# Optimization experiments

Measured on AMD Instinct MI355X. Metric: run time of the kernel, lower is better.

## Reference

```python
import jax, jax.numpy as jnp
import numpy as np
import math

B, S, HID = 1, 4096, 2048
NH, NKV, DH = 8, 1, 256
ROPE_BASE = 10000.0


def setup_inputs() -> dict:
    key = jax.random.key(0)
    ks = jax.random.split(key, 5)
    sc = 0.02
    return {
        "hidden_states": jax.random.normal(ks[0], (B, S, HID), dtype=jnp.float32),
        "position_ids": jnp.arange(S, dtype=jnp.int32)[None, :].repeat(B, axis=0),
        "wq": jax.random.normal(ks[1], (HID, NH * DH), dtype=jnp.float32) * sc,
        "wk": jax.random.normal(ks[2], (HID, NKV * DH), dtype=jnp.float32) * sc,
        "wv": jax.random.normal(ks[3], (HID, NKV * DH), dtype=jnp.float32) * sc,
        "wo": jax.random.normal(ks[4], (NH * DH, HID), dtype=jnp.float32) * sc,
    }


def _rope_cos_sin(position_ids, dtype):
    # inv_freq: [DH/2]
    inv_freq = 1.0 / (ROPE_BASE ** (jnp.arange(0, DH, 2, dtype=jnp.float32) / DH))
    # freqs: [B, S, DH/2]
    freqs = position_ids.astype(jnp.float32)[:, :, None] * inv_freq[None, None, :]
    emb = jnp.concatenate([freqs, freqs], axis=-1)  # [B, S, DH]
    return jnp.cos(emb).astype(dtype), jnp.sin(emb).astype(dtype)


def _rotate_half(x):
    x1, x2 = x[..., : DH // 2], x[..., DH // 2 :]
    return jnp.concatenate([-x2, x1], axis=-1)


def reference(hidden_states, position_ids, wq, wk, wv, wo):
    bsz, q_len, _ = hidden_states.shape
    dtype = hidden_states.dtype

    # QKV projections (bias=False)
    q = (hidden_states @ wq).reshape(bsz, q_len, NH, DH).transpose(0, 2, 1, 3)   # [B,NH,S,DH]
    k = (hidden_states @ wk).reshape(bsz, q_len, NKV, DH).transpose(0, 2, 1, 3)  # [B,NKV,S,DH]
    v = (hidden_states @ wv).reshape(bsz, q_len, NKV, DH).transpose(0, 2, 1, 3)  # [B,NKV,S,DH]

    # RoPE (unsqueeze_dim=1 -> broadcast over heads)
    cos, sin = _rope_cos_sin(position_ids, dtype)
    cos, sin = cos[:, None, :, :], sin[:, None, :, :]  # [B,1,S,DH]
    q = q * cos + _rotate_half(q) * sin
    k = k * cos + _rotate_half(k) * sin

    # GQA: k/v broadcast over the NH head dim via matmul broadcasting (repeat_kv)
    scores = jnp.matmul(q, jnp.swapaxes(k, -1, -2)) / math.sqrt(DH)  # [B,NH,S,S]

    # additive causal mask (0 on/below diagonal, -inf-ish above)
    neg = jnp.finfo(jnp.float32).min
    causal = jnp.where(
        jnp.tril(jnp.ones((q_len, q_len), dtype=bool)), 0.0, neg
    ).astype(jnp.float32)[None, None, :, :]
    scores = scores + causal

    probs = jax.nn.softmax(scores.astype(jnp.float32), axis=-1).astype(dtype)
    attn = jnp.matmul(probs, v)  # [B,NH,S,DH] (v broadcasts over NH)

    attn = attn.transpose(0, 2, 1, 3).reshape(bsz, q_len, NH * DH)
    return attn @ wo
```

## Files before the change

### kernel.cpp

```cpp
#include <hip/hip_runtime.h>
#include <hip/hip_bf16.h>

typedef __bf16 bf16;
typedef __attribute__((ext_vector_type(8))) __bf16 bf16x8;
typedef __attribute__((ext_vector_type(4))) float f32x4;

#define S_LEN  4096
#define HIDDEN 2048
#define N_HEADS 8
#define D_HEAD 256
#define QKV_N  2560
#define NEG_BIG (-1e30f)
#define MFIX 8.0f

#define OFF_WQKVT 0u
#define OFF_WOT   10485760u
#define OFF_QKV   18874368u
#define OFF_VT    39845888u
#define OFF_AOUT  41943040u
#define OFF_FLAG  58720256u
#define WS_NEED   58720320u
#define OFF_PBUF  0u
#define OFF_LBUF  8388608u

__global__ __launch_bounds__(256) void detect_dtype(const unsigned short* __restrict__ w,
                                                    int* __restrict__ flag) {
  __shared__ int bad;
  if (threadIdx.x == 0) bad = 0;
  __syncthreads();
  int local = 0;
  for (int i = threadIdx.x; i < 4096; i += 256) {
    int e = (w[i] >> 7) & 0xFF;
    if (e >= 130) local = 1;
  }
  if (local) atomicOr(&bad, 1);
  __syncthreads();
  if (threadIdx.x == 0) *flag = bad;
}

__device__ __forceinline__ bf16x8 load8(const void* p, size_t idx, bool f32) {
  if (f32) {
    const float* q = (const float*)p + idx;
    bf16x8 r;
#pragma unroll
    for (int j = 0; j < 8; ++j) r[j] = (bf16)q[j];
    return r;
  }
  return *(const bf16x8*)((const bf16*)p + idx);
}

__global__ __launch_bounds__(256) void cvt_hs(const void* __restrict__ hs,
                                              bf16* __restrict__ dst,
                                              const int* __restrict__ flag) {
  bool f32 = (*flag != 0);
  size_t i = ((size_t)blockIdx.x * 256 + threadIdx.x) * 8;
  *(bf16x8*)(dst + i) = load8(hs, i, f32);
}

__device__ __forceinline__ void transpose_tile64(const void* __restrict__ src, size_t sbase,
                                                 int sld, bool f32,
                                                 bf16* __restrict__ dst, int dld,
                                                 bf16 (*T)[72]) {
  int tid = threadIdx.x;
  int r  = tid >> 2;
  int c4 = (tid & 3) * 16;
  *(bf16x8*)(&T[r][c4])     = load8(src, sbase + (size_t)r * sld + c4, f32);
  *(bf16x8*)(&T[r][c4 + 8]) = load8(src, sbase + (size_t)r * sld + c4 + 8, f32);
  __syncthreads();
  bf16x8 v0, v1;
#pragma unroll
  for (int j = 0; j < 8; ++j) { v0[j] = T[c4 + j][r]; v1[j] = T[c4 + 8 + j][r]; }
  *(bf16x8*)(dst + (size_t)r * dld + c4)     = v0;
  *(bf16x8*)(dst + (size_t)r * dld + c4 + 8) = v1;
}

__global__ __launch_bounds__(256) void build_wqkvT(const void* __restrict__ wq,
                                                   const void* __restrict__ wk,
                                                   const void* __restrict__ wv,
                                                   bf16* __restrict__ dst,
                                                   const int* __restrict__ flag) {
  __shared__ __align__(16) bf16 T[64][72];
  bool f32 = (*flag != 0);
  int n0 = blockIdx.x * 64;
  int k0 = blockIdx.y * 64;
  const void* src; int ld, c0;
  if (n0 < 2048)      { src = wq; ld = 2048; c0 = n0; }
  else if (n0 < 2304) { src = wk; ld = 256;  c0 = n0 - 2048; }
  else                { src = wv; ld = 256;  c0 = n0 - 2304; }
  transpose_tile64(src, (size_t)k0 * ld + c0, ld, f32,
                   dst + (size_t)n0 * HIDDEN + k0, HIDDEN, T);
}

__global__ __launch_bounds__(256) void transpose_any(const void* __restrict__ src, int sbase,
                                                     int sld,
                                                     bf16* __restrict__ dst, int dld,
                                                     const int* __restrict__ flag) {
  __shared__ __align__(16) bf16 T[64][72];
  bool f32 = flag && (*flag != 0);
  int c0 = blockIdx.x * 64;
  int r0 = blockIdx.y * 64;
  transpose_tile64(src, (size_t)sbase + (size_t)r0 * sld + c0, sld, f32,
                   dst + (size_t)c0 * dld + r0, dld, T);
}

__device__ __forceinline__ void gload16(const bf16* g, bf16* l) {
  __builtin_amdgcn_global_load_lds((__attribute__((address_space(1))) void*)(void*)g,
                                   (__attribute__((address_space(3))) void*)(void*)l,
                                   16, 0, 0);
}

__global__ __launch_bounds__(256) void gemm_bk64(const bf16* __restrict__ A,
                                                 const bf16* __restrict__ BT,
                                                 void* __restrict__ C,
                                                 int M, int N, int K,
                                                 const int* __restrict__ cflag) {
  __shared__ __align__(16) bf16 As[2][128 * 64];
  __shared__ __align__(16) bf16 Bs[2][128 * 64];
  bool cf32 = cflag && (*cflag != 0);
  int tid  = threadIdx.x;
  int w = tid >> 6, lane = tid & 63;
  int quad = lane >> 4, l16 = lane & 15;

  int nx = gridDim.x;
  int nwg = nx * gridDim.y;
  int bid = blockIdx.y * nx + blockIdx.x;
  int swz = (bid & 7) * (nwg >> 3) + (bid >> 3);
  int bm = (swz / nx) * 128, bn = (swz % nx) * 128;
  int wm = (w >> 1) * 64, wn = (w & 1) * 64;

  int lr = lane >> 3, lc = lane & 7;
  int scol = ((lc ^ lr) << 3);
  const bf16* Ag[4]; const bf16* Bg[4];
#pragma unroll
  for (int j = 0; j < 4; ++j) {
    int row = (w * 4 + j) * 8 + lr;
    Ag[j] = A  + (size_t)(bm + row) * K + scol;
    Bg[j] = BT + (size_t)(bn + row) * K + scol;
  }

  int nIter = K >> 6;
#pragma unroll
  for (int j = 0; j < 4; ++j) {
    gload16(Ag[j], &As[0][(w * 4 + j) * 512]);
    gload16(Bg[j], &Bs[0][(w * 4 + j) * 512]);
  }
  __syncthreads();

  int cA = ((quad    ) ^ (l16 & 7)) << 3;
  int cB = ((quad + 4) ^ (l16 & 7)) << 3;

  f32x4 acc[4][4] = {};
  for (int kt = 0; kt < nIter; ++kt) {
    int cur = kt & 1;
    if (kt + 1 < nIter) {
      int nxt = cur ^ 1;
      int koff = (kt + 1) << 6;
#pragma unroll
      for (int j = 0; j < 4; ++j) {
        gload16(Ag[j] + koff, &As[nxt][(w * 4 + j) * 512]);
        gload16(Bg[j] + koff, &Bs[nxt][(w * 4 + j) * 512]);
      }
    }
    const bf16* Ab = &As[cur][0];
    const bf16* Bb = &Bs[cur][0];
#pragma unroll
    for (int h = 0; h < 2; ++h) {
      int cc = h ? cB : cA;
      bf16x8 af[4], bfr[4];
#pragma unroll
      for (int mt = 0; mt < 4; ++mt)
        af[mt] = *(const bf16x8*)(Ab + (wm + mt * 16 + l16) * 64 + cc);
#pragma unroll
      for (int nt = 0; nt < 4; ++nt)
        bfr[nt] = *(const bf16x8*)(Bb + (wn + nt * 16 + l16) * 64 + cc);
#pragma unroll
      for (int mt = 0; mt < 4; ++mt)
#pragma unroll
        for (int nt = 0; nt < 4; ++nt)
          acc[mt][nt] = __builtin_amdgcn_mfma_f32_16x16x32_bf16(af[mt], bfr[nt],
                                                                acc[mt][nt], 0, 0, 0);
    }
    __syncthreads();
  }

#pragma unroll
  for (int mt = 0; mt < 4; ++mt)
#pragma unroll
    for (int nt = 0; nt < 4; ++nt)
#pragma unroll
      for (int r = 0; r < 4; ++r) {
        int row = bm + wm + mt * 16 + quad * 4 + r;
        int col = bn + wn + nt * 16 + l16;
        size_t off = (size_t)row * N + col;
        float v = acc[mt][nt][r];
        if (cf32) ((float*)C)[off] = v;
        else      ((bf16*)C)[off] = (bf16)v;
      }
}

__global__ __launch_bounds__(256) void rope_kernel(bf16* __restrict__ qkv,
                                                   const int* __restrict__ pos) {
  int s = blockIdx.x;
  float p = (float)pos[s];
  bf16* row = qkv + (size_t)s * QKV_N;
  for (int i = threadIdx.x; i < 9 * 128; i += 256) {
    int h = i >> 7, d = i & 127;
    float inv = __expf(-(float)d * (9.210340371976184f / 128.0f));
    float th = p * inv;
    float sn, c;
    sincosf(th, &sn, &c);
    c  = (float)(bf16)c;
    sn = (float)(bf16)sn;
    bf16* x = row + ((h < 8) ? h * 256 : 2048);
    float x1 = (float)x[d], x2 = (float)x[d + 128];
    x[d]       = (bf16)(x1 * c - x2 * sn);
    x[d + 128] = (bf16)(x2 * c + x1 * sn);
  }
}

__device__ __forceinline__ void stage_kv(const bf16* __restrict__ qkv,
                                         const bf16* __restrict__ VT,
                                         bf16* __restrict__ kb, bf16* __restrict__ vb,
                                         int kv0, int w, int lane) {
#pragma unroll
  for (int i = 0; i < 4; ++i) {
    int seg = w * 4 + i;
    int rK = seg * 2 + (lane >> 5);
    int sK = (lane & 31) ^ (rK & 31);
    gload16(qkv + (size_t)(kv0 + rK) * QKV_N + 2048 + sK * 8, kb + seg * 512);
    int rV = seg * 8 + (lane >> 3);
    int sV = (lane & 7) ^ (rV & 7);
    gload16(VT + (size_t)rV * S_LEN + kv0 + sV * 8, vb + seg * 512);
  }
}

__global__ __launch_bounds__(512, 2) void attn_kernel(const bf16* __restrict__ qkv,
                                                      const bf16* __restrict__ VT,
                                                      bf16* __restrict__ aout,
                                                      bf16* __restrict__ pbuf,
                                                      float* __restrict__ lbuf) {
  __shared__ __align__(16) bf16 Ks[2][64 * 256];
  __shared__ __align__(16) bf16 Vs[2][256 * 64];
  __shared__ __align__(16) bf16 Pl[8][16][72];
  int tid  = threadIdx.x;
  int w = tid >> 6, lane = tid & 63;
  int quad = lane >> 4, l16 = lane & 15;
  int bx   = blockIdx.x;
  int head = bx & 7;
  int t    = bx >> 3;
  int a    = t & 15, which = t >> 4;
  int qBig = 31 - a;
  int tilesBig = 2 * qBig + 2;

  int nseg, sqt[2], sk0[2], sk1[2], smode[2];
  if (which == 0) {
    nseg = 1; sqt[0] = qBig; sk0[0] = 0;  sk1[0] = 33;        smode[0] = 1;
  } else {
    nseg = 2;
    sqt[0] = qBig; sk0[0] = 33; sk1[0] = tilesBig;  smode[0] = 2;
    sqt[1] = a;    sk0[1] = 0;  sk1[1] = 2 * a + 2; smode[1] = 0;
  }
  int pidx = head * 16 + a;

  for (int sg = 0; sg < nseg; ++sg) {
    int qt = sqt[sg], k0 = sk0[sg], k1 = sk1[sg], mode = smode[sg];
    int qrow_w = qt * 128 + w * 16;

    const bf16* qrow = qkv + (size_t)(qrow_w + l16) * QKV_N + head * D_HEAD + quad * 8;
    bf16x8 qf[8];
#pragma unroll
    for (int dc = 0; dc < 8; ++dc) {
      bf16x8 tq = *(const bf16x8*)(qrow + dc * 32);
#pragma unroll
      for (int j = 0; j < 8; ++j) tq[j] = (bf16)((float)tq[j] * 0.0625f);
      qf[dc] = tq;
    }

    f32x4 o[16] = {};
    float lsum[4] = {0.f, 0.f, 0.f, 0.f};

    __syncthreads();
    stage_kv(qkv, VT, Ks[0], Vs[0], k0 << 6, w, lane);

    for (int kt = k0; kt < k1; ++kt) {
      int par = (kt - k0) & 1;
      __syncthreads();
      if (kt + 1 < k1)
        stage_kv(qkv, VT, Ks[par ^ 1], Vs[par ^ 1], (kt + 1) << 6, w, lane);

      f32x4 sv[4] = {};
      __builtin_amdgcn_s_setprio(1);
#pragma unroll
      for (int dc = 0; dc < 8; ++dc)
#pragma unroll
        for (int n = 0; n < 4; ++n) {
          int row = n * 16 + l16;
          bf16x8 kf = *(const bf16x8*)(Ks[par] + row * 256 +
                                       (((dc << 2) + quad) ^ (row & 31)) * 8);
          sv[n] = __builtin_amdgcn_mfma_f32_16x16x32_bf16(qf[dc], kf, sv[n], 0, 0, 0);
        }
      __builtin_amdgcn_s_setprio(0);

      bool dg = (kt * 64 + 63) > qrow_w;
      float pv4[4][4];
#pragma unroll
      for (int n = 0; n < 4; ++n)
#pragma unroll
        for (int r = 0; r < 4; ++r) {
          float x = sv[n][r] - MFIX;
          if (dg && (kt * 64 + n * 16 + l16 > qrow_w + quad * 4 + r)) x = NEG_BIG;
          float e = __expf(x);
          pv4[n][r] = e;
          lsum[r] += e;
        }
#pragma unroll
      for (int n = 0; n < 4; ++n)
#pragma unroll
        for (int r = 0; r < 4; ++r)
          Pl[w][quad * 4 + r][n * 16 + l16] = (bf16)pv4[n][r];
      asm volatile("s_waitcnt lgkmcnt(0)" ::: "memory");
      bf16x8 pa0 = *(const bf16x8*)(&Pl[w][l16][quad * 8]);
      bf16x8 pa1 = *(const bf16x8*)(&Pl[w][l16][32 + quad * 8]);

      __builtin_amdgcn_s_setprio(1);
#pragma unroll
      for (int dt = 0; dt < 16; ++dt) {
        int row = dt * 16 + l16;
        const bf16* vb2 = Vs[par] + row * 64;
        bf16x8 v0 = *(const bf16x8*)(vb2 + ((quad)     ^ (row & 7)) * 8);
        bf16x8 v1 = *(const bf16x8*)(vb2 + ((4 + quad) ^ (row & 7)) * 8);
        o[dt] = __builtin_amdgcn_mfma_f32_16x16x32_bf16(pa0, v0, o[dt], 0, 0, 0);
        o[dt] = __builtin_amdgcn_mfma_f32_16x16x32_bf16(pa1, v1, o[dt], 0, 0, 0);
      }
      __builtin_amdgcn_s_setprio(0);
    }

    float lrow[4];
#pragma unroll
    for (int r = 0; r < 4; ++r) lrow[r] = lsum[r];
#pragma unroll
    for (int off = 8; off >= 1; off >>= 1)
#pragma unroll
      for (int r = 0; r < 4; ++r)
        lrow[r] += __shfl_xor(lrow[r], off, 16);
    int rowb = w * 16 + quad * 4;

    if (mode == 0) {
      float invl[4];
#pragma unroll
      for (int r = 0; r < 4; ++r) invl[r] = 1.0f / lrow[r];
      bf16* orow = aout + (size_t)(qt * 128 + rowb) * HIDDEN + head * D_HEAD + l16;
#pragma unroll
      for (int dt = 0; dt < 16; ++dt)
#pragma unroll
        for (int r = 0; r < 4; ++r)
          orow[(size_t)r * HIDDEN + dt * 16] = (bf16)(o[dt][r] * invl[r]);
    } else {
      if (mode == 1) {
        bf16* orow = aout + (size_t)(qt * 128 + rowb) * HIDDEN + head * D_HEAD + l16;
#pragma unroll
        for (int dt = 0; dt < 16; ++dt)
#pragma unroll
          for (int r = 0; r < 4; ++r)
            orow[(size_t)r * HIDDEN + dt * 16] = (bf16)o[dt][r];
      } else {
        bf16* orow = pbuf + ((size_t)pidx * 128 + rowb) * 256 + l16;
#pragma unroll
        for (int dt = 0; dt < 16; ++dt)
#pragma unroll
          for (int r = 0; r < 4; ++r)
            orow[(size_t)r * 256 + dt * 16] = (bf16)o[dt][r];
      }
      if (l16 == 0) {
        int base = (pidx * 2 + which) * 128 + rowb;
#pragma unroll
        for (int r = 0; r < 4; ++r) lbuf[base + r] = lrow[r];
      }
    }
  }
}

__global__ __launch_bounds__(256) void combine_kernel(bf16* __restrict__ aout,
                                                      const bf16* __restrict__ pbuf,
                                                      const float* __restrict__ lbuf) {
  int p = blockIdx.x;
  int h = p >> 4, a = p & 15;
  int qBig = 31 - a;
  int tid = threadIdx.x;
  for (int i = tid; i < 4096; i += 256) {
    int rowin = i >> 5;
    int d8 = (i & 31) * 8;
    float l = lbuf[(p * 2 + 0) * 128 + rowin] + lbuf[(p * 2 + 1) * 128 + rowin];
    float inv = 1.0f / l;
    bf16* ap = aout + (size_t)(qBig * 128 + rowin) * HIDDEN + h * D_HEAD + d8;
    const bf16* bp = pbuf + ((size_t)p * 128 + rowin) * 256 + d8;
    bf16x8 va = *(const bf16x8*)ap;
    bf16x8 vb = *(const bf16x8*)bp;
    bf16x8 vo;
#pragma unroll
    for (int j = 0; j < 8; ++j)
      vo[j] = (bf16)(((float)va[j] + (float)vb[j]) * inv);
    *(bf16x8*)ap = vo;
  }
}

extern "C" void kernel_launch(void* const* d_in, const int* in_sizes, int n_in,
                              void* d_out, int out_size, void* d_ws, size_t ws_size,
                              hipStream_t stream) {
  if (ws_size < (size_t)WS_NEED) return;
  const void* hs  = d_in[0];
  const int*  pos = (const int*)d_in[1];
  const void* wq  = d_in[2];
  const void* wk  = d_in[3];
  const void* wv  = d_in[4];
  const void* wo  = d_in[5];

  char* ws = (char*)d_ws;
  bf16* wqkvT = (bf16*)(ws + OFF_WQKVT);
  bf16* woT   = (bf16*)(ws + OFF_WOT);
  bf16* qkv   = (bf16*)(ws + OFF_QKV);
  bf16* VT    = (bf16*)(ws + OFF_VT);
  bf16* aout  = (bf16*)(ws + OFF_AOUT);
  int*  flag  = (int*)(ws + OFF_FLAG);
  bf16*  pbuf = (bf16*)(ws + OFF_PBUF);
  float* lbuf = (float*)(ws + OFF_LBUF);
  bf16*  hsb  = aout;

  detect_dtype<<<1, 256, 0, stream>>>((const unsigned short*)wq, flag);
  build_wqkvT<<<dim3(QKV_N / 64, HIDDEN / 64), 256, 0, stream>>>(wq, wk, wv, wqkvT, flag);
  transpose_any<<<dim3(HIDDEN / 64, HIDDEN / 64), 256, 0, stream>>>(wo, 0, HIDDEN,
                                                                    woT, HIDDEN, flag);
  cvt_hs<<<(S_LEN * HIDDEN) / (256 * 8), 256, 0, stream>>>(hs, hsb, flag);
  gemm_bk64<<<dim3(QKV_N / 128, S_LEN / 128), 256, 0, stream>>>(hsb, wqkvT, qkv,
                                                                S_LEN, QKV_N, HIDDEN,
                                                                nullptr);
  rope_kernel<<<S_LEN, 256, 0, stream>>>(qkv, pos);
  transpose_any<<<dim3(D_HEAD / 64, S_LEN / 64), 256, 0, stream>>>(qkv, 2304, QKV_N,
                                                                   VT, S_LEN, nullptr);
  attn_kernel<<<N_HEADS * 32, 512, 0, stream>>>(qkv, VT, aout, pbuf, lbuf);
  combine_kernel<<<128, 256, 0, stream>>>(aout, pbuf, lbuf);
  gemm_bk64<<<dim3(HIDDEN / 128, S_LEN / 128), 256, 0, stream>>>(aout, woT, d_out,
                                                                 S_LEN, HIDDEN, HIDDEN,
                                                                 flag);
}
```

Before: 353.8 us.

## Split KV tile across warp halves with 32-row Q per warp and LDS reduction

Each warp now handles 32 query rows (two 16-row groups) and half of the 64-key KV tile, instead of 16 rows over the full tile. Each K/V fragment read from LDS therefore feeds two MFMAs, halving LDS fragment traffic per MFMA. The two halves' partial outputs and row sums are combined at the end through shared memory. This doubles the accumulator registers, which risks spills or lower occupancy under launch_bounds(512,2), and adds a cross-warp reduction with extra syncthreads.

```diff
diff --git a/kernel.cpp b/kernel.cpp
--- a/kernel.cpp
+++ b/kernel.cpp
@@ -241,10 +241,11 @@
                                                       float* __restrict__ lbuf) {
   __shared__ __align__(16) bf16 Ks[2][64 * 256];
   __shared__ __align__(16) bf16 Vs[2][256 * 64];
-  __shared__ __align__(16) bf16 Pl[8][16][72];
+  __shared__ __align__(16) bf16 Pl[8][32][40];
   int tid  = threadIdx.x;
   int w = tid >> 6, lane = tid & 63;
   int quad = lane >> 4, l16 = lane & 15;
+  int w4 = w & 3, half = w >> 2;
   int bx   = blockIdx.x;
   int head = bx & 7;
   int t    = bx >> 3;
@@ -264,20 +265,23 @@
 
   for (int sg = 0; sg < nseg; ++sg) {
     int qt = sqt[sg], k0 = sk0[sg], k1 = sk1[sg], mode = smode[sg];
-    int qrow_w = qt * 128 + w * 16;
-
-    const bf16* qrow = qkv + (size_t)(qrow_w + l16) * QKV_N + head * D_HEAD + quad * 8;
-    bf16x8 qf[8];
-#pragma unroll
-    for (int dc = 0; dc < 8; ++dc) {
-      bf16x8 tq = *(const bf16x8*)(qrow + dc * 32);
-#pragma unroll
-      for (int j = 0; j < 8; ++j) tq[j] = (bf16)((float)tq[j] * 0.0625f);
-      qf[dc] = tq;
+    int qrow_w = qt * 128 + w4 * 32;
+
+    bf16x8 qf[2][8];
+#pragma unroll
+    for (int g = 0; g < 2; ++g) {
+      const bf16* qr = qkv + (size_t)(qrow_w + g * 16 + l16) * QKV_N + head * D_HEAD + quad * 8;
+#pragma unroll
+      for (int dc = 0; dc < 8; ++dc) {
+        bf16x8 tq = *(const bf16x8*)(qr + dc * 32);
+#pragma unroll
+        for (int j = 0; j < 8; ++j) tq[j] = (bf16)((float)tq[j] * 0.0625f);
+        qf[g][dc] = tq;
+      }
     }
 
-    f32x4 o[16] = {};
-    float lsum[4] = {0.f, 0.f, 0.f, 0.f};
+    f32x4 o[2][16] = {};
+    float lsum[2][4] = {};
 
     __syncthreads();
     stage_kv(qkv, VT, Ks[0], Vs[0], k0 << 6, w, lane);
@@ -288,93 +292,147 @@
       if (kt + 1 < k1)
         stage_kv(qkv, VT, Ks[par ^ 1], Vs[par ^ 1], (kt + 1) << 6, w, lane);
 
-      f32x4 sv[4] = {};
+      f32x4 sv[2][2] = {};
       __builtin_amdgcn_s_setprio(1);
 #pragma unroll
       for (int dc = 0; dc < 8; ++dc)
 #pragma unroll
-        for (int n = 0; n < 4; ++n) {
-          int row = n * 16 + l16;
+        for (int n = 0; n < 2; ++n) {
+          int row = half * 32 + n * 16 + l16;
           bf16x8 kf = *(const bf16x8*)(Ks[par] + row * 256 +
                                        (((dc << 2) + quad) ^ (row & 31)) * 8);
-          sv[n] = __builtin_amdgcn_mfma_f32_16x16x32_bf16(qf[dc], kf, sv[n], 0, 0, 0);
+          sv[0][n] = __builtin_amdgcn_mfma_f32_16x16x32_bf16(qf[0][dc], kf, sv[0][n], 0, 0, 0);
+          sv[1][n] = __builtin_amdgcn_mfma_f32_16x16x32_bf16(qf[1][dc], kf, sv[1][n], 0, 0, 0);
         }
       __builtin_amdgcn_s_setprio(0);
 
-      bool dg = (kt * 64 + 63) > qrow_w;
-      float pv4[4][4];
-#pragma unroll
-      for (int n = 0; n < 4; ++n)
-#pragma unroll
-        for (int r = 0; r < 4; ++r) {
-          float x = sv[n][r] - MFIX;
-          if (dg && (kt * 64 + n * 16 + l16 > qrow_w + quad * 4 + r)) x = NEG_BIG;
-          float e = __expf(x);
-          pv4[n][r] = e;
-          lsum[r] += e;
-        }
-#pragma unroll
-      for (int n = 0; n < 4; ++n)
-#pragma unroll
-        for (int r = 0; r < 4; ++r)
-          Pl[w][quad * 4 + r][n * 16 + l16] = (bf16)pv4[n][r];
+      int kvb = kt * 64 + half * 32;
+      bool dg = (kvb + 31) > qrow_w;
+#pragma unroll
+      for (int g = 0; g < 2; ++g)
+#pragma unroll
+        for (int n = 0; n < 2; ++n)
+#pragma unroll
+          for (int r = 0; r < 4; ++r) {
+            float x = sv[g][n][r] - MFIX;
+            if (dg && (kvb + n * 16 + l16 > qrow_w + g * 16 + quad * 4 + r)) x = NEG_BIG;
+            float e = __expf(x);
+            lsum[g][r] += e;
+            Pl[w][g * 16 + quad * 4 + r][n * 16 + l16] = (bf16)e;
+          }
       asm volatile("s_waitcnt lgkmcnt(0)" ::: "memory");
       bf16x8 pa0 = *(const bf16x8*)(&Pl[w][l16][quad * 8]);
-      bf16x8 pa1 = *(const bf16x8*)(&Pl[w][l16][32 + quad * 8]);
+      bf16x8 pa1 = *(const bf16x8*)(&Pl[w][16 + l16][quad * 8]);
 
       __builtin_amdgcn_s_setprio(1);
 #pragma unroll
       for (int dt = 0; dt < 16; ++dt) {
         int row = dt * 16 + l16;
-        const bf16* vb2 = Vs[par] + row * 64;
-        bf16x8 v0 = *(const bf16x8*)(vb2 + ((quad)     ^ (row & 7)) * 8);
-        bf16x8 v1 = *(const bf16x8*)(vb2 + ((4 + quad) ^ (row & 7)) * 8);
-        o[dt] = __builtin_amdgcn_mfma_f32_16x16x32_bf16(pa0, v0, o[dt], 0, 0, 0);
-        o[dt] = __builtin_amdgcn_mfma_f32_16x16x32_bf16(pa1, v1, o[dt], 0, 0, 0);
+        bf16x8 vf = *(const bf16x8*)(Vs[par] + row * 64 +
+                                     (((half << 2) + quad) ^ (row & 7)) * 8);
+        o[0][dt] = __builtin_amdgcn_mfma_f32_16x16x32_bf16(pa0, vf, o[0][dt], 0, 0, 0);
+        o[1][dt] = __builtin_amdgcn_mfma_f32_16x16x32_bf16(pa1, vf, o[1][dt], 0, 0, 0);
       }
       __builtin_amdgcn_s_setprio(0);
     }
 
-    float lrow[4];
-#pragma unroll
-    for (int r = 0; r < 4; ++r) lrow[r] = lsum[r];
+    float lrow[2][4];
+#pragma unroll
+    for (int g = 0; g < 2; ++g)
+#pragma unroll
+      for (int r = 0; r < 4; ++r) lrow[g][r] = lsum[g][r];
 #pragma unroll
     for (int off = 8; off >= 1; off >>= 1)
 #pragma unroll
-      for (int r = 0; r < 4; ++r)
-        lrow[r] += __shfl_xor(lrow[r], off, 16);
-    int rowb = w * 16 + quad * 4;
-
-    if (mode == 0) {
-      float invl[4];
-#pragma unroll
-      for (int r = 0; r < 4; ++r) invl[r] = 1.0f / lrow[r];
-      bf16* orow = aout + (size_t)(qt * 128 + rowb) * HIDDEN + head * D_HEAD + l16;
-#pragma unroll
-      for (int dt = 0; dt < 16; ++dt)
+      for (int g = 0; g < 2; ++g)
 #pragma unroll
         for (int r = 0; r < 4; ++r)
-          orow[(size_t)r * HIDDEN + dt * 16] = (bf16)(o[dt][r] * invl[r]);
-    } else {
-      if (mode == 1) {
-        bf16* orow = aout + (size_t)(qt * 128 + rowb) * HIDDEN + head * D_HEAD + l16;
+          lrow[g][r] += __shfl_xor(lrow[g][r], off, 16);
+
+    __syncthreads();
+    float* ob  = (w4 < 2) ? ((float*)Ks + w4 * 8192) : ((float*)Vs + (w4 - 2) * 8192);
+    float* lsh = (float*)Pl;
+    if (half == 1) {
+#pragma unroll
+      for (int g = 0; g < 2; ++g)
 #pragma unroll
         for (int dt = 0; dt < 16; ++dt)
 #pragma unroll
+          for (int r = 0; r < 4; ++r) {
+            int qr = g * 16 + quad * 4 + r;
+            ob[qr * 256 + ((dt * 16 + l16 + 4 * qr) & 255)] = o[g][dt][r];
+          }
+      if (l16 == 0) {
+#pragma unroll
+        for (int g = 0; g < 2; ++g)
+#pragma unroll
           for (int r = 0; r < 4; ++r)
-            orow[(size_t)r * HIDDEN + dt * 16] = (bf16)o[dt][r];
+            lsh[w4 * 32 + g * 16 + quad * 4 + r] = lrow[g][r];
+      }
+    }
+    __syncthreads();
+    if (half == 0) {
+#pragma unroll
+      for (int g = 0; g < 2; ++g)
+#pragma unroll
+        for (int dt = 0; dt < 16; ++dt)
+#pragma unroll
+          for (int r = 0; r < 4; ++r) {
+            int qr = g * 16 + quad * 4 + r;
+            o[g][dt][r] += ob[qr * 256 + ((dt * 16 + l16 + 4 * qr) & 255)];
+          }
+#pragma unroll
+      for (int g = 0; g < 2; ++g)
+#pragma unroll
+        for (int r = 0; r < 4; ++r)
+          lrow[g][r] += lsh[w4 * 32 + g * 16 + quad * 4 + r];
+
+      int rowb0 = w4 * 32;
+      if (mode == 0) {
+#pragma unroll
+        for (int g = 0; g < 2; ++g) {
+          float invl[4];
+#pragma unroll
+          for (int r = 0; r < 4; ++r) invl[r] = 1.0f / lrow[g][r];
+          bf16* orow = aout + (size_t)(qt * 128 + rowb0 + g * 16 + quad * 4) * HIDDEN
+                       + head * D_HEAD + l16;
+#pragma unroll
+          for (int dt = 0; dt < 16; ++dt)
+#pragma unroll
+            for (int r = 0; r < 4; ++r)
+              orow[(size_t)r * HIDDEN + dt * 16] = (bf16)(o[g][dt][r] * invl[r]);
+        }
       } else {
-        bf16* orow = pbuf + ((size_t)pidx * 128 + rowb) * 256 + l16;
-#pragma unroll
-        for (int dt = 0; dt < 16; ++dt)
-#pragma unroll
-          for (int r = 0; r < 4; ++r)
-            orow[(size_t)r * 256 + dt * 16] = (bf16)o[dt][r];
-      }
-      if (l16 == 0) {
-        int base = (pidx * 2 + which) * 128 + rowb;
-#pragma unroll
-        for (int r = 0; r < 4; ++r) lbuf[base + r] = lrow[r];
+        if (mode == 1) {
+#pragma unroll
+          for (int g = 0; g < 2; ++g) {
+            bf16* orow = aout + (size_t)(qt * 128 + rowb0 + g * 16 + quad * 4) * HIDDEN
+                         + head * D_HEAD + l16;
+#pragma unroll
+            for (int dt = 0; dt < 16; ++dt)
+#pragma unroll
+              for (int r = 0; r < 4; ++r)
+                orow[(size_t)r * HIDDEN + dt * 16] = (bf16)o[g][dt][r];
+          }
+        } else {
+#pragma unroll
+          for (int g = 0; g < 2; ++g) {
+            bf16* orow = pbuf + ((size_t)pidx * 128 + rowb0 + g * 16 + quad * 4) * 256 + l16;
+#pragma unroll
+            for (int dt = 0; dt < 16; ++dt)
+#pragma unroll
+              for (int r = 0; r < 4; ++r)
+                orow[(size_t)r * 256 + dt * 16] = (bf16)o[g][dt][r];
+          }
+        }
+        if (l16 == 0) {
+#pragma unroll
+          for (int g = 0; g < 2; ++g) {
+            int base = (pidx * 2 + which) * 128 + rowb0 + g * 16 + quad * 4;
+#pragma unroll
+            for (int r = 0; r < 4; ++r) lbuf[base + r] = lrow[g][r];
+          }
+        }
       }
     }
   }
```

Result: slower. 451.8 us (+27.7%).

## Single-buffer GEMM LDS and read V directly from global in attention

Applied to the files above, without the earlier changes.

The GEMM drops its double-buffered LDS prefetch for a single buffer with load-then-sync per K step, so global loads no longer overlap MFMA work. The attention kernel stops staging V tiles into shared memory and has each wave read V fragments straight from global (transposed V) inside the PV loop, halving LDS use. This may raise occupancy, but it exposes global-load latency in both the GEMM and the PV inner loop, and the 8 waves re-read the same V from global/L2.

```diff
diff --git a/kernel.cpp b/kernel.cpp
--- a/kernel.cpp
+++ b/kernel.cpp
@@ -114,8 +114,8 @@
                                                  void* __restrict__ C,
                                                  int M, int N, int K,
                                                  const int* __restrict__ cflag) {
-  __shared__ __align__(16) bf16 As[2][128 * 64];
-  __shared__ __align__(16) bf16 Bs[2][128 * 64];
+  __shared__ __align__(16) bf16 As[128 * 64];
+  __shared__ __align__(16) bf16 Bs[128 * 64];
   bool cf32 = cflag && (*cflag != 0);
   int tid  = threadIdx.x;
   int w = tid >> 6, lane = tid & 63;
@@ -138,41 +138,30 @@
     Bg[j] = BT + (size_t)(bn + row) * K + scol;
   }
 
-  int nIter = K >> 6;
-#pragma unroll
-  for (int j = 0; j < 4; ++j) {
-    gload16(Ag[j], &As[0][(w * 4 + j) * 512]);
-    gload16(Bg[j], &Bs[0][(w * 4 + j) * 512]);
-  }
-  __syncthreads();
-
   int cA = ((quad    ) ^ (l16 & 7)) << 3;
   int cB = ((quad + 4) ^ (l16 & 7)) << 3;
 
+  int nIter = K >> 6;
   f32x4 acc[4][4] = {};
   for (int kt = 0; kt < nIter; ++kt) {
-    int cur = kt & 1;
-    if (kt + 1 < nIter) {
-      int nxt = cur ^ 1;
-      int koff = (kt + 1) << 6;
-#pragma unroll
-      for (int j = 0; j < 4; ++j) {
-        gload16(Ag[j] + koff, &As[nxt][(w * 4 + j) * 512]);
-        gload16(Bg[j] + koff, &Bs[nxt][(w * 4 + j) * 512]);
-      }
+    int koff = kt << 6;
+    __syncthreads();
+#pragma unroll
+    for (int j = 0; j < 4; ++j) {
+      gload16(Ag[j] + koff, &As[(w * 4 + j) * 512]);
+      gload16(Bg[j] + koff, &Bs[(w * 4 + j) * 512]);
     }
-    const bf16* Ab = &As[cur][0];
-    const bf16* Bb = &Bs[cur][0];
+    __syncthreads();
 #pragma unroll
     for (int h = 0; h < 2; ++h) {
       int cc = h ? cB : cA;
       bf16x8 af[4], bfr[4];
 #pragma unroll
       for (int mt = 0; mt < 4; ++mt)
-        af[mt] = *(const bf16x8*)(Ab + (wm + mt * 16 + l16) * 64 + cc);
+        af[mt] = *(const bf16x8*)(As + (wm + mt * 16 + l16) * 64 + cc);
 #pragma unroll
       for (int nt = 0; nt < 4; ++nt)
-        bfr[nt] = *(const bf16x8*)(Bb + (wn + nt * 16 + l16) * 64 + cc);
+        bfr[nt] = *(const bf16x8*)(Bs + (wn + nt * 16 + l16) * 64 + cc);
 #pragma unroll
       for (int mt = 0; mt < 4; ++mt)
 #pragma unroll
@@ -180,7 +169,6 @@
           acc[mt][nt] = __builtin_amdgcn_mfma_f32_16x16x32_bf16(af[mt], bfr[nt],
                                                                 acc[mt][nt], 0, 0, 0);
     }
-    __syncthreads();
   }
 
 #pragma unroll
@@ -218,19 +206,15 @@
   }
 }
 
-__device__ __forceinline__ void stage_kv(const bf16* __restrict__ qkv,
-                                         const bf16* __restrict__ VT,
-                                         bf16* __restrict__ kb, bf16* __restrict__ vb,
-                                         int kv0, int w, int lane) {
+__device__ __forceinline__ void stage_k(const bf16* __restrict__ qkv,
+                                        bf16* __restrict__ kb,
+                                        int kv0, int w, int lane) {
 #pragma unroll
   for (int i = 0; i < 4; ++i) {
     int seg = w * 4 + i;
     int rK = seg * 2 + (lane >> 5);
     int sK = (lane & 31) ^ (rK & 31);
     gload16(qkv + (size_t)(kv0 + rK) * QKV_N + 2048 + sK * 8, kb + seg * 512);
-    int rV = seg * 8 + (lane >> 3);
-    int sV = (lane & 7) ^ (rV & 7);
-    gload16(VT + (size_t)rV * S_LEN + kv0 + sV * 8, vb + seg * 512);
   }
 }
 
@@ -240,7 +224,6 @@
                                                       bf16* __restrict__ pbuf,
                                                       float* __restrict__ lbuf) {
   __shared__ __align__(16) bf16 Ks[2][64 * 256];
-  __shared__ __align__(16) bf16 Vs[2][256 * 64];
   __shared__ __align__(16) bf16 Pl[8][16][72];
   int tid  = threadIdx.x;
   int w = tid >> 6, lane = tid & 63;
@@ -280,13 +263,14 @@
     float lsum[4] = {0.f, 0.f, 0.f, 0.f};
 
     __syncthreads();
-    stage_kv(qkv, VT, Ks[0], Vs[0], k0 << 6, w, lane);
+    stage_k(qkv, Ks[0], k0 << 6, w, lane);
 
     for (int kt = k0; kt < k1; ++kt) {
       int par = (kt - k0) & 1;
+      int kv0 = kt << 6;
       __syncthreads();
       if (kt + 1 < k1)
-        stage_kv(qkv, VT, Ks[par ^ 1], Vs[par ^ 1], (kt + 1) << 6, w, lane);
+        stage_k(qkv, Ks[par ^ 1], (kt + 1) << 6, w, lane);
 
       f32x4 sv[4] = {};
       __builtin_amdgcn_s_setprio(1);
@@ -301,14 +285,14 @@
         }
       __builtin_amdgcn_s_setprio(0);
 
-      bool dg = (kt * 64 + 63) > qrow_w;
+      bool dg = (kv0 + 63) > qrow_w;
       float pv4[4][4];
 #pragma unroll
       for (int n = 0; n < 4; ++n)
 #pragma unroll
         for (int r = 0; r < 4; ++r) {
           float x = sv[n][r] - MFIX;
-          if (dg && (kt * 64 + n * 16 + l16 > qrow_w + quad * 4 + r)) x = NEG_BIG;
+          if (dg && (kv0 + n * 16 + l16 > qrow_w + quad * 4 + r)) x = NEG_BIG;
           float e = __expf(x);
           pv4[n][r] = e;
           lsum[r] += e;
@@ -322,13 +306,13 @@
       bf16x8 pa0 = *(const bf16x8*)(&Pl[w][l16][quad * 8]);
       bf16x8 pa1 = *(const bf16x8*)(&Pl[w][l16][32 + quad * 8]);
 
+      const bf16* vbase = VT + (size_t)l16 * S_LEN + kv0 + quad * 8;
       __builtin_amdgcn_s_setprio(1);
 #pragma unroll
       for (int dt = 0; dt < 16; ++dt) {
-        int row = dt * 16 + l16;
-        const bf16* vb2 = Vs[par] + row * 64;
-        bf16x8 v0 = *(const bf16x8*)(vb2 + ((quad)     ^ (row & 7)) * 8);
-        bf16x8 v1 = *(const bf16x8*)(vb2 + ((4 + quad) ^ (row & 7)) * 8);
+        const bf16* vg = vbase + (size_t)dt * 16 * S_LEN;
+        bf16x8 v0 = *(const bf16x8*)(vg);
+        bf16x8 v1 = *(const bf16x8*)(vg + 32);
         o[dt] = __builtin_amdgcn_mfma_f32_16x16x32_bf16(pa0, v0, o[dt], 0, 0, 0);
         o[dt] = __builtin_amdgcn_mfma_f32_16x16x32_bf16(pa1, v1, o[dt], 0, 0, 0);
       }
```

Measured after the change: 563.8 us. +59.4%, slower.
